# Kernel optimization log

Measured on AMD Instinct MI355X. Metric: run time of the kernel, lower is better.

## Reference

```python
import jax, jax.numpy as jnp
import numpy as np

NB = 5  # frequency bands


def _ln(x, g, b, eps=1e-5):
    m = jnp.mean(x, axis=-1, keepdims=True)
    v = jnp.var(x, axis=-1, keepdims=True)
    return (x - m) / jnp.sqrt(v + eps) * g + b


def _graph_adj(x, adj_w, sw1, sb1, sw2, sb2, pos_factor, pos_enc):
    # x: [B, D, N] -> degree-normalized adjacency [B, N, N]
    d = x.shape[1]
    xt = jnp.swapaxes(x, 1, 2)  # [B, N, D]
    # concat-MLP first layer split: cat(xi, xj) @ W1 == xi @ W1[:d] + xj @ W1[d:]
    a = xt @ sw1[:d]
    bpart = xt @ sw1[d:]
    h = jax.nn.elu(a[:, :, None, :] + bpart[:, None, :, :] + sb1)  # [B, N, N, H]
    dyn = jax.nn.sigmoid(jnp.squeeze(h @ sw2, -1) + sb2)  # [B, N, N]
    static = jax.nn.softmax(adj_w, axis=-1)
    pos = jax.nn.softmax(pos_enc, axis=-1)
    comb = jax.nn.softmax(static + dyn + pos_factor * pos, axis=-1)
    deg = jnp.sum(comb, axis=-1)
    dis = (deg + 1e-8) ** -0.5
    return dis[:, :, None] * comb * dis[:, None, :]


def _gcn(x, adj, w, b):
    # x: [B, D, N], adj: [B, N, N] -> [B, D_out, N]
    xt = jnp.swapaxes(x, 1, 2)
    out = jnp.einsum('bij,bjd->bid', adj, xt) @ w + b
    return jnp.swapaxes(out, 1, 2)


def _mha(x, qkv_w, qkv_b, ow, ob, nh=4):
    B, S, D = x.shape
    dh = D // nh
    q, k, v = jnp.split(x @ qkv_w + qkv_b, 3, axis=-1)
    q = q.reshape(B, S, nh, dh)
    k = k.reshape(B, S, nh, dh)
    v = v.reshape(B, S, nh, dh)
    att = jax.nn.softmax(jnp.einsum('bihd,bjhd->bhij', q, k) / float(np.sqrt(dh)), axis=-1)
    o = jnp.einsum('bhij,bjhd->bihd', att, v).reshape(B, S, D)
    return o @ ow + ob


def setup_inputs():
    key = jax.random.key(0)
    B, D, N = 16, 256, 64
    ks = iter(jax.random.split(key, 40))

    def rn(shape, s=0.05):
        return jax.random.normal(next(ks), shape, dtype=jnp.float32) * s

    eyeN = jnp.eye(N, dtype=jnp.float32)
    return dict(
        feature=jax.random.normal(next(ks), (B, NB * D, 1, N), dtype=jnp.float32),
        l_adj_w=jnp.tile(eyeN[None], (NB, 1, 1)),
        l_sim_w1=rn((NB, 2 * D, D)), l_sim_b1=jnp.zeros((NB, D), jnp.float32),
        l_sim_w2=rn((NB, D, 1)), l_sim_b2=jnp.zeros((NB, 1), jnp.float32),
        l_pos_factor=jnp.full((NB,), 0.5, jnp.float32),
        l_pos_enc=jnp.tile(eyeN[None], (NB, 1, 1)),
        l_gcn_w=rn((NB, D, D)), l_gcn_b=jnp.zeros((NB, D), jnp.float32),
        g_adj_w=jnp.eye(NB, dtype=jnp.float32),
        g_sim_w1=rn((2 * D, D)), g_sim_b1=jnp.zeros((D,), jnp.float32),
        g_sim_w2=rn((D, 1)), g_sim_b2=jnp.zeros((1,), jnp.float32),
        g_pos_factor=jnp.float32(0.5),
        g_pos_enc=jnp.eye(NB, dtype=jnp.float32),
        g_gcn_w=rn((D, D)), g_gcn_b=jnp.zeros((D,), jnp.float32),
        qkv_w=rn((D, 3 * D)), qkv_b=jnp.zeros((3 * D,), jnp.float32),
        attn_ow=rn((D, D)), attn_ob=jnp.zeros((D,), jnp.float32),
        ln1_g=jnp.ones((D,), jnp.float32), ln1_b=jnp.zeros((D,), jnp.float32),
        ln2_g=jnp.ones((D,), jnp.float32), ln2_b=jnp.zeros((D,), jnp.float32),
        mlp_w1=rn((D, 4 * D)), mlp_b1=jnp.zeros((4 * D,), jnp.float32),
        mlp_w2=rn((4 * D, D)), mlp_b2=jnp.zeros((D,), jnp.float32),
        imp_w=rn((NB, N, 1)), imp_b=jnp.zeros((NB, 1), jnp.float32),
    )


def reference(feature, l_adj_w, l_sim_w1, l_sim_b1, l_sim_w2, l_sim_b2,
              l_pos_factor, l_pos_enc, l_gcn_w, l_gcn_b,
              g_adj_w, g_sim_w1, g_sim_b1, g_sim_w2, g_sim_b2,
              g_pos_factor, g_pos_enc, g_gcn_w, g_gcn_b,
              qkv_w, qkv_b, attn_ow, attn_ob,
              ln1_g, ln1_b, ln2_g, ln2_b,
              mlp_w1, mlp_b1, mlp_w2, mlp_b2,
              imp_w, imp_b):
    B = feature.shape[0]
    D = l_gcn_w.shape[-1]
    N = feature.shape[-1]
    # [B, 5*D, 1, N] -> [5, B, D, N] band-major
    x5 = jnp.moveaxis(feature.reshape(B, NB, D, N), 1, 0)
    # per-band local graphs + GCNs (vmapped over the 5 bands)
    local_adj = jax.vmap(_graph_adj)(x5, l_adj_w, l_sim_w1, l_sim_b1,
                                     l_sim_w2, l_sim_b2, l_pos_factor, l_pos_enc)
    local_out = jax.vmap(_gcn)(x5, local_adj, l_gcn_w, l_gcn_b)  # [5, B, D, N]
    scale_nodes = jnp.moveaxis(jnp.mean(local_out, axis=-1), 0, 1)  # [B, 5, D]
    # cross-band attention block (pre: MHA + residual + LN, then MLP + residual + LN)
    attn = _mha(scale_nodes, qkv_w, qkv_b, attn_ow, attn_ob)
    h1 = _ln(scale_nodes + attn, ln1_g, ln1_b)
    mlp = jax.nn.gelu(h1 @ mlp_w1 + mlp_b1, approximate=False) @ mlp_w2 + mlp_b2
    se = _ln(h1 + mlp, ln2_g, ln2_b)  # [B, 5, D]
    # global scale graph over the 5 band nodes
    xg = jnp.swapaxes(se, 1, 2)  # [B, D, 5]
    g_adj = _graph_adj(xg, g_adj_w, g_sim_w1, g_sim_b1, g_sim_w2, g_sim_b2,
                       g_pos_factor, g_pos_enc)
    g_out = jnp.swapaxes(_gcn(xg, g_adj, g_gcn_w, g_gcn_b), 1, 2)  # [B, 5, D]
    # modulate each local band feature by its global scale vector
    enh = local_out * jnp.moveaxis(g_out, 1, 0)[..., None]  # [5, B, D, N]
    # per-band importance projection over channels: [5, B, D, 1]
    out5 = jnp.einsum('kbdn,kno->kbdo', enh, imp_w) + imp_b[:, None, None, :]
    output = jnp.moveaxis(out5, 0, 1).reshape(B, NB * D, 1, 1)
    return output, g_adj, jnp.moveaxis(local_out, 0, 1)
```

## Files before the change

### kernel.cpp

```cpp
#include <hip/hip_runtime.h>
#include <hip/hip_bf16.h>

#define NBANDS 5
#define BATCH  16
#define DIM    256
#define NNODE  64
#define SEQ    5

typedef __hip_bfloat16 bf16;
typedef unsigned short ushort_t;
typedef __attribute__((ext_vector_type(8))) short short8;
typedef __attribute__((ext_vector_type(4))) float float4v;

#define MFMA __builtin_amdgcn_mfma_f32_16x16x32_bf16

__device__ __forceinline__ float bu2f(ushort_t u){
    bf16 h = *reinterpret_cast<bf16*>(&u);
    return __bfloat162float(h);
}
__device__ __forceinline__ ushort_t f2bu(float x){
    bf16 h = __float2bfloat16(x);
    return *reinterpret_cast<ushort_t*>(&h);
}
__device__ __forceinline__ float elu(float v){
    return (v > 0.f) ? v : (__expf(v) - 1.f);
}

__global__ void __launch_bounds__(256) k_head(
    const float* __restrict__ l_adj_w, const float* __restrict__ l_pos_enc,
    const float* __restrict__ l_pf,
    const float* __restrict__ g_adj_w, const float* __restrict__ g_pos_enc,
    const float* __restrict__ g_pf,
    float* __restrict__ sbase, float* __restrict__ gbase,
    const float* __restrict__ w1, const float* __restrict__ gw,
    ushort_t* __restrict__ w1bt, ushort_t* __restrict__ gwbt)
{
    int blk = blockIdx.x;
    int tid = threadIdx.x;
    __shared__ ushort_t tile[64][65];

    if (blk < 80) {
        int r = blk*4 + (tid>>6);
        int k = r >> 6, i = r & 63;
        int t = tid & 63;
        float aw = l_adj_w[(k*NNODE + i)*NNODE + t];
        float pe = l_pos_enc[(k*NNODE + i)*NNODE + t];
        float m1 = aw, m2 = pe;
        for (int o=32;o>0;o>>=1){ m1 = fmaxf(m1, __shfl_xor(m1,o,64)); m2 = fmaxf(m2, __shfl_xor(m2,o,64)); }
        float e1 = __expf(aw-m1), e2 = __expf(pe-m2);
        float s1=e1, s2=e2;
        for (int o=32;o>0;o>>=1){ s1 += __shfl_xor(s1,o,64); s2 += __shfl_xor(s2,o,64); }
        float pf = l_pf[k];
        sbase[(k*NNODE+i)*NNODE + t] = e1/s1 + pf*(e2/s2);
    } else if (blk == 80) {
        if (tid < NBANDS) {
            int i = tid;
            float r1[NBANDS], r2[NBANDS];
            float m1=-1e30f, m2=-1e30f;
            for (int j=0;j<NBANDS;j++){
                r1[j]=g_adj_w[i*NBANDS+j]; r2[j]=g_pos_enc[i*NBANDS+j];
                m1=fmaxf(m1,r1[j]); m2=fmaxf(m2,r2[j]);
            }
            float s1=0.f,s2=0.f;
            for (int j=0;j<NBANDS;j++){ r1[j]=__expf(r1[j]-m1); r2[j]=__expf(r2[j]-m2); s1+=r1[j]; s2+=r2[j]; }
            float pf = g_pf[0];
            for (int j=0;j<NBANDS;j++) gbase[i*NBANDS+j] = r1[j]/s1 + pf*(r2[j]/s2);
        }
    } else {
        int idx = blk - 81;
        int inst = idx >> 4;
        int t = idx & 15;
        int r0 = (t>>2)*64, c0 = (t&3)*64;
        const float* src; ushort_t* dst;
        if (inst < 10){
            int k = inst>>1, half = inst&1;
            src = w1  + ((size_t)k*512 + half*256)*256;
            dst = w1bt+ ((size_t)k*512 + half*256)*256;
        } else {
            int k = inst-10;
            src = gw  + (size_t)k*65536;
            dst = gwbt+ (size_t)k*65536;
        }
        int jj = tid & 63, i4 = tid >> 6;
        for (int p=0;p<16;p++){
            int i = p*4 + i4;
            tile[i][jj] = f2bu(src[(size_t)(r0+i)*256 + c0 + jj]);
        }
        __syncthreads();
        for (int p=0;p<16;p++){
            int i = p*4 + i4;
            dst[(size_t)(c0+i)*256 + r0 + jj] = tile[jj][i];
        }
    }
}

__global__ void __launch_bounds__(512) k_graph(
    const float* __restrict__ feat,
    const ushort_t* __restrict__ w1bt, const float* __restrict__ b1,
    const float* __restrict__ w2, const float* __restrict__ b2arr,
    const float* __restrict__ sbase,
    const ushort_t* __restrict__ gwbt, const float* __restrict__ gb,
    const float* __restrict__ imp_w,
    float* __restrict__ out_local,
    float* __restrict__ scalew4, float* __restrict__ impw4)
{
    int k  = blockIdx.x >> 6;
    int b  = (blockIdx.x >> 2) & 15;
    int iq = blockIdx.x & 3;
    int i0 = iq << 4;
    int tid = threadIdx.x;
    int w = tid >> 6, lane = tid & 63, c16 = lane & 15, quad = lane >> 4;

    __shared__ union {
        ushort_t xtb[64][264];
        ushort_t ab[80][264];
    } U;
    __shared__ ushort_t cs[16][72];
    __shared__ ushort_t ys[16][264];
    __shared__ float w2s[DIM];

    const float* src = feat + ((size_t)b*NBANDS + k)*DIM*NNODE;

    if (tid < DIM) w2s[tid] = w2[k*DIM + tid];
    #pragma unroll
    for (int u = 0; u < 32; ++u){
        int idx = u*512 + tid;
        U.xtb[idx & 63][idx >> 6] = f2bu(src[idx]);
    }
    __syncthreads();

    int col0 = w*32 + c16;
    int col1 = col0 + 16;

    const ushort_t* Ba = w1bt + (size_t)k*512*DIM;
    const ushort_t* Bb = Ba + 256*DIM;
    float4v z = {0.f,0.f,0.f,0.f};
    float4v aA0=z, aA1=z;
    float4v aB00=z,aB01=z,aB10=z,aB11=z,aB20=z,aB21=z,aB30=z,aB31=z;
    #pragma unroll
    for (int ks = 0; ks < 8; ++ks){
        int ko = ks*32 + quad*8;
        short8 fa = *reinterpret_cast<const short8*>(&U.xtb[i0 + c16][ko]);
        short8 f0 = *reinterpret_cast<const short8*>(&U.xtb[ 0 + c16][ko]);
        short8 f1 = *reinterpret_cast<const short8*>(&U.xtb[16 + c16][ko]);
        short8 f2 = *reinterpret_cast<const short8*>(&U.xtb[32 + c16][ko]);
        short8 f3 = *reinterpret_cast<const short8*>(&U.xtb[48 + c16][ko]);
        short8 wa0 = *reinterpret_cast<const short8*>(Ba + (size_t)col0*DIM + ko);
        short8 wa1 = *reinterpret_cast<const short8*>(Ba + (size_t)col1*DIM + ko);
        short8 wb0 = *reinterpret_cast<const short8*>(Bb + (size_t)col0*DIM + ko);
        short8 wb1 = *reinterpret_cast<const short8*>(Bb + (size_t)col1*DIM + ko);
        aA0  = MFMA(fa, wa0, aA0, 0,0,0);
        aA1  = MFMA(fa, wa1, aA1, 0,0,0);
        aB00 = MFMA(f0, wb0, aB00, 0,0,0);
        aB01 = MFMA(f0, wb1, aB01, 0,0,0);
        aB10 = MFMA(f1, wb0, aB10, 0,0,0);
        aB11 = MFMA(f1, wb1, aB11, 0,0,0);
        aB20 = MFMA(f2, wb0, aB20, 0,0,0);
        aB21 = MFMA(f2, wb1, aB21, 0,0,0);
        aB30 = MFMA(f3, wb0, aB30, 0,0,0);
        aB31 = MFMA(f3, wb1, aB31, 0,0,0);
    }
    __syncthreads();
    {
        float bias0 = b1[k*DIM + col0];
        float bias1 = b1[k*DIM + col1];
        int r0 = quad*4;
        #pragma unroll
        for (int r = 0; r < 4; ++r){
            U.ab[r0 + r][col0]      = f2bu(aA0[r] + bias0);
            U.ab[r0 + r][col1]      = f2bu(aA1[r] + bias1);
            U.ab[16 + r0 + r][col0] = f2bu(aB00[r]);
            U.ab[16 + r0 + r][col1] = f2bu(aB01[r]);
            U.ab[32 + r0 + r][col0] = f2bu(aB10[r]);
            U.ab[32 + r0 + r][col1] = f2bu(aB11[r]);
            U.ab[48 + r0 + r][col0] = f2bu(aB20[r]);
            U.ab[48 + r0 + r][col1] = f2bu(aB21[r]);
            U.ab[64 + r0 + r][col0] = f2bu(aB30[r]);
            U.ab[64 + r0 + r][col1] = f2bu(aB31[r]);
        }
    }
    __syncthreads();

    {
        int il0 = w*2, il1 = w*2 + 1;
        float acc0 = 0.f, acc1 = 0.f;
        const ushort_t* ar0 = U.ab[il0];
        const ushort_t* ar1 = U.ab[il1];
        const ushort_t* br  = U.ab[16 + lane];
        #pragma unroll 4
        for (int dd = 0; dd < 64; ++dd){
            ushort4 bv = *reinterpret_cast<const ushort4*>(br  + dd*4);
            ushort4 a0 = *reinterpret_cast<const ushort4*>(ar0 + dd*4);
            ushort4 a1 = *reinterpret_cast<const ushort4*>(ar1 + dd*4);
            float4 wv  = *reinterpret_cast<const float4*>(&w2s[dd*4]);
            float bx = bu2f(bv.x), by = bu2f(bv.y), bz = bu2f(bv.z), bq = bu2f(bv.w);
            acc0 += elu(bu2f(a0.x)+bx)*wv.x + elu(bu2f(a0.y)+by)*wv.y
                  + elu(bu2f(a0.z)+bz)*wv.z + elu(bu2f(a0.w)+bq)*wv.w;
            acc1 += elu(bu2f(a1.x)+bx)*wv.x + elu(bu2f(a1.y)+by)*wv.y
                  + elu(bu2f(a1.z)+bz)*wv.z + elu(bu2f(a1.w)+bq)*wv.w;
        }
        float sb2 = b2arr[k];
        float sg0 = 1.f/(1.f + __expf(-(acc0 + sb2)));
        float sg1 = 1.f/(1.f + __expf(-(acc1 + sb2)));
        float val0 = sbase[(k*NNODE + i0 + il0)*NNODE + lane] + sg0;
        float val1 = sbase[(k*NNODE + i0 + il1)*NNODE + lane] + sg1;
        float m0 = val0, m1 = val1;
        for (int o=32;o>0;o>>=1){ m0 = fmaxf(m0, __shfl_xor(m0,o,64)); m1 = fmaxf(m1, __shfl_xor(m1,o,64)); }
        float e0 = __expf(val0 - m0), e1 = __expf(val1 - m1);
        float s0 = e0, s1 = e1;
        for (int o=32;o>0;o>>=1){ s0 += __shfl_xor(s0,o,64); s1 += __shfl_xor(s1,o,64); }
        cs[il0][lane] = f2bu(e0/s0);
        cs[il1][lane] = f2bu(e1/s1);
    }
    __syncthreads();

    {
        float4v aY0 = z, aY1 = z;
        #pragma unroll
        for (int ks = 0; ks < 2; ++ks){
            int ko = ks*32 + quad*8;
            short8 af = *reinterpret_cast<const short8*>(&cs[c16][ko]);
            const float* f0p = src + (size_t)col0*NNODE + ko;
            const float* f1p = src + (size_t)col1*NNODE + ko;
            float4 x0 = *reinterpret_cast<const float4*>(f0p);
            float4 x1 = *reinterpret_cast<const float4*>(f0p+4);
            float4 y0 = *reinterpret_cast<const float4*>(f1p);
            float4 y1 = *reinterpret_cast<const float4*>(f1p+4);
            short8 bf0, bf1;
            bf0[0]=(short)f2bu(x0.x); bf0[1]=(short)f2bu(x0.y); bf0[2]=(short)f2bu(x0.z); bf0[3]=(short)f2bu(x0.w);
            bf0[4]=(short)f2bu(x1.x); bf0[5]=(short)f2bu(x1.y); bf0[6]=(short)f2bu(x1.z); bf0[7]=(short)f2bu(x1.w);
            bf1[0]=(short)f2bu(y0.x); bf1[1]=(short)f2bu(y0.y); bf1[2]=(short)f2bu(y0.z); bf1[3]=(short)f2bu(y0.w);
            bf1[4]=(short)f2bu(y1.x); bf1[5]=(short)f2bu(y1.y); bf1[6]=(short)f2bu(y1.z); bf1[7]=(short)f2bu(y1.w);
            aY0 = MFMA(af, bf0, aY0, 0,0,0);
            aY1 = MFMA(af, bf1, aY1, 0,0,0);
        }
        #pragma unroll
        for (int r=0;r<4;++r){
            ys[quad*4 + r][col0] = f2bu(aY0[r]);
            ys[quad*4 + r][col1] = f2bu(aY1[r]);
        }
    }
    __syncthreads();

    {
        float4v aG0 = z, aG1 = z;
        const ushort_t* Bg = gwbt + (size_t)k*DIM*DIM;
        #pragma unroll
        for (int ks = 0; ks < 8; ++ks){
            int ko = ks*32 + quad*8;
            short8 af = *reinterpret_cast<const short8*>(&ys[c16][ko]);
            short8 g0 = *reinterpret_cast<const short8*>(Bg + (size_t)col0*DIM + ko);
            short8 g1 = *reinterpret_cast<const short8*>(Bg + (size_t)col1*DIM + ko);
            aG0 = MFMA(af, g0, aG0, 0,0,0);
            aG1 = MFMA(af, g1, aG1, 0,0,0);
        }
        int nb = i0 + quad*4;
        float iw0 = imp_w[k*NNODE + nb + 0];
        float iw1 = imp_w[k*NNODE + nb + 1];
        float iw2 = imp_w[k*NNODE + nb + 2];
        float iw3 = imp_w[k*NNODE + nb + 3];
        size_t obase = ((size_t)b*NBANDS + k)*DIM;

        float bias0 = gb[k*DIM + col0];
        float v0 = aG0[0]+bias0, v1 = aG0[1]+bias0, v2 = aG0[2]+bias0, v3 = aG0[3]+bias0;
        float4 vv = make_float4(v0,v1,v2,v3);
        *reinterpret_cast<float4*>(&out_local[(obase + col0)*NNODE + nb]) = vv;
        float s  = v0+v1+v2+v3;
        float di = v0*iw0 + v1*iw1 + v2*iw2 + v3*iw3;
        s  += __shfl_xor(s,16,64);  s  += __shfl_xor(s,32,64);
        di += __shfl_xor(di,16,64); di += __shfl_xor(di,32,64);
        if (quad == 0){
            size_t o = ((size_t)iq*80 + b*SEQ + k)*DIM + col0;
            scalew4[o] = s;
            impw4[o]   = di;
        }

        float bias1 = gb[k*DIM + col1];
        v0 = aG1[0]+bias1; v1 = aG1[1]+bias1; v2 = aG1[2]+bias1; v3 = aG1[3]+bias1;
        vv = make_float4(v0,v1,v2,v3);
        *reinterpret_cast<float4*>(&out_local[(obase + col1)*NNODE + nb]) = vv;
        s  = v0+v1+v2+v3;
        di = v0*iw0 + v1*iw1 + v2*iw2 + v3*iw3;
        s  += __shfl_xor(s,16,64);  s  += __shfl_xor(s,32,64);
        di += __shfl_xor(di,16,64); di += __shfl_xor(di,32,64);
        if (quad == 0){
            size_t o = ((size_t)iq*80 + b*SEQ + k)*DIM + col1;
            scalew4[o] = s;
            impw4[o]   = di;
        }
    }
}

__device__ __forceinline__ void ln_row(float* row, const float* g, const float* bb, int lane)
{
    float v0 = row[lane], v1 = row[lane+64], v2 = row[lane+128], v3 = row[lane+192];
    float s = v0+v1+v2+v3;
    for (int o=32;o>0;o>>=1) s += __shfl_xor(s,o,64);
    float mean = s * (1.f/256.f);
    float c0 = v0-mean, c1 = v1-mean, c2 = v2-mean, c3 = v3-mean;
    float q = c0*c0+c1*c1+c2*c2+c3*c3;
    for (int o=32;o>0;o>>=1) q += __shfl_xor(q,o,64);
    float rs = rsqrtf(q*(1.f/256.f) + 1e-5f);
    row[lane]     = c0*rs*g[lane]     + bb[lane];
    row[lane+64]  = c1*rs*g[lane+64]  + bb[lane+64];
    row[lane+128] = c2*rs*g[lane+128] + bb[lane+128];
    row[lane+192] = c3*rs*g[lane+192] + bb[lane+192];
}

__global__ void __launch_bounds__(1024) k_tail(
    const float* __restrict__ scalew4, const float* __restrict__ impw4,
    const float* __restrict__ qkv_w, const float* __restrict__ qkv_b,
    const float* __restrict__ attn_ow, const float* __restrict__ attn_ob,
    const float* __restrict__ ln1_g, const float* __restrict__ ln1_b,
    const float* __restrict__ mlp_w1, const float* __restrict__ mlp_b1,
    const float* __restrict__ mlp_w2, const float* __restrict__ mlp_b2,
    const float* __restrict__ ln2_g, const float* __restrict__ ln2_b,
    const float* __restrict__ gw1, const float* __restrict__ gb1,
    const float* __restrict__ gw2, const float* __restrict__ gb2,
    const float* __restrict__ gbase,
    const float* __restrict__ ggw, const float* __restrict__ ggb,
    const float* __restrict__ imp_b,
    float* __restrict__ out0, float* __restrict__ out_gadj)
{
    int b = blockIdx.x;
    int tid = threadIdx.x;
    int w = tid >> 6, lane = tid & 63;

    __shared__ __align__(16) float A[5160];
    __shared__ __align__(16) float Bp[5200];
    __shared__ __align__(16) float C[1300];
    __shared__ __align__(16) float Dx[1300];
    __shared__ __align__(16) float E[1300];
    __shared__ float F[64];

    #pragma unroll
    for (int p = 0; p < 2; ++p){
        int id = tid + p*1024;
        if (id < SEQ*DIM){
            int i = id >> 8, d = id & 255;
            size_t base = ((size_t)b*SEQ + i)*DIM + d;
            float v = scalew4[base] + scalew4[20480 + base]
                    + scalew4[40960 + base] + scalew4[61440 + base];
            C[i*260 + d] = v * (1.f/64.f);
        }
    }
    __syncthreads();

    if (tid < 768){
        int n = tid;
        float bias = qkv_b[n];
        float acc[5] = {bias,bias,bias,bias,bias};
        for (int d = 0; d < DIM; d += 4){
            float wv0 = qkv_w[(size_t)d*768 + n];
            float wv1 = qkv_w[(size_t)(d+1)*768 + n];
            float wv2 = qkv_w[(size_t)(d+2)*768 + n];
            float wv3 = qkv_w[(size_t)(d+3)*768 + n];
            #pragma unroll
            for (int i=0;i<5;++i){
                float4 cv = *reinterpret_cast<const float4*>(&C[i*260 + d]);
                acc[i] += cv.x*wv0 + cv.y*wv1 + cv.z*wv2 + cv.w*wv3;
            }
        }
        #pragma unroll
        for (int i=0;i<5;++i) A[i*772 + n] = acc[i];
    }
    __syncthreads();

    for (int p = w; p < 20; p += 16){
        int i = p >> 2, h = p & 3;
        float qv = A[i*772 + h*64 + lane];
        float pj[SEQ];
        #pragma unroll
        for (int j=0;j<SEQ;++j){
            float x = qv * A[j*772 + 256 + h*64 + lane];
            for (int o=32;o>0;o>>=1) x += __shfl_xor(x,o,64);
            pj[j] = x * 0.125f;
        }
        float m = pj[0];
        #pragma unroll
        for (int j=1;j<SEQ;++j) m = fmaxf(m, pj[j]);
        float ss = 0.f;
        #pragma unroll
        for (int j=0;j<SEQ;++j){ pj[j] = __expf(pj[j]-m); ss += pj[j]; }
        float inv = 1.f/ss;
        float o = 0.f;
        #pragma unroll
        for (int j=0;j<SEQ;++j) o += pj[j]*inv * A[j*772 + 512 + h*64 + lane];
        Dx[i*260 + h*64 + lane] = o;
    }
    __syncthreads();

    if (tid < DIM){
        int n = tid;
        float bias = attn_ob[n];
        float acc[5] = {bias,bias,bias,bias,bias};
        for (int d = 0; d < DIM; d += 4){
            float wv0 = attn_ow[(size_t)d*DIM + n];
            float wv1 = attn_ow[(size_t)(d+1)*DIM + n];
            float wv2 = attn_ow[(size_t)(d+2)*DIM + n];
            float wv3 = attn_ow[(size_t)(d+3)*DIM + n];
            #pragma unroll
            for (int i=0;i<5;++i){
                float4 xv = *reinterpret_cast<const float4*>(&Dx[i*260 + d]);
                acc[i] += xv.x*wv0 + xv.y*wv1 + xv.z*wv2 + xv.w*wv3;
            }
        }
        #pragma unroll
        for (int i=0;i<5;++i) E[i*260 + n] = C[i*260 + n] + acc[i];
    }
    __syncthreads();
    if (w < SEQ) ln_row(&E[w*260], ln1_g, ln1_b, lane);
    __syncthreads();

    {
        int m = tid;
        float bias = mlp_b1[m];
        float acc[5] = {bias,bias,bias,bias,bias};
        for (int d = 0; d < DIM; d += 4){
            float wv0 = mlp_w1[(size_t)d*1024 + m];
            float wv1 = mlp_w1[(size_t)(d+1)*1024 + m];
            float wv2 = mlp_w1[(size_t)(d+2)*1024 + m];
            float wv3 = mlp_w1[(size_t)(d+3)*1024 + m];
            #pragma unroll
            for (int i=0;i<5;++i){
                float4 xv = *reinterpret_cast<const float4*>(&E[i*260 + d]);
                acc[i] += xv.x*wv0 + xv.y*wv1 + xv.z*wv2 + xv.w*wv3;
            }
        }
        #pragma unroll
        for (int i=0;i<5;++i){
            float v = acc[i];
            A[i*1032 + m] = 0.5f*v*(1.f + erff(v*0.70710678118654752f));
        }
    }
    __syncthreads();

    {
        int n = tid & 255, s = tid >> 8;
        float acc[5] = {0.f,0.f,0.f,0.f,0.f};
        const float* wbase = mlp_w2 + (size_t)s*256*DIM + n;
        const float* mbase = A + s*256;
        for (int kk = 0; kk < 256; kk += 4){
            float wv0 = wbase[(size_t)kk*DIM];
            float wv1 = wbase[(size_t)(kk+1)*DIM];
            float wv2 = wbase[(size_t)(kk+2)*DIM];
            float wv3 = wbase[(size_t)(kk+3)*DIM];
            #pragma unroll
            for (int i=0;i<5;++i){
                float4 xv = *reinterpret_cast<const float4*>(&mbase[i*1032 + kk]);
                acc[i] += xv.x*wv0 + xv.y*wv1 + xv.z*wv2 + xv.w*wv3;
            }
        }
        #pragma unroll
        for (int i=0;i<5;++i) Bp[(s*5 + i)*260 + n] = acc[i];
    }
    __syncthreads();
    if (tid < DIM){
        int n = tid;
        float b2v = mlp_b2[n];
        #pragma unroll
        for (int i=0;i<5;++i){
            float m2 = b2v + Bp[i*260+n] + Bp[(5+i)*260+n] + Bp[(10+i)*260+n] + Bp[(15+i)*260+n];
            C[i*260 + n] = m2 + E[i*260 + n];
        }
    }
    __syncthreads();
    if (w < SEQ) ln_row(&C[w*260], ln2_g, ln2_b, lane);
    __syncthreads();

    {
        int n = tid & 255, s = tid >> 8;
        int mat = s >> 1, half = s & 1;
        float acc[5] = {0.f,0.f,0.f,0.f,0.f};
        const float* wbase = gw1 + ((size_t)mat*DIM + half*128)*DIM + n;
        for (int kk = 0; kk < 128; kk += 4){
            int d = half*128 + kk;
            float wv0 = wbase[(size_t)kk*DIM];
            float wv1 = wbase[(size_t)(kk+1)*DIM];
            float wv2 = wbase[(size_t)(kk+2)*DIM];
            float wv3 = wbase[(size_t)(kk+3)*DIM];
            #pragma unroll
            for (int i=0;i<5;++i){
                float4 xv = *reinterpret_cast<const float4*>(&C[i*260 + d]);
                acc[i] += xv.x*wv0 + xv.y*wv1 + xv.z*wv2 + xv.w*wv3;
            }
        }
        #pragma unroll
        for (int i=0;i<5;++i) Bp[(s*5 + i)*260 + n] = acc[i];
    }
    __syncthreads();
    if (tid < DIM){
        int n = tid;
        float g1v = gb1[n];
        #pragma unroll
        for (int i=0;i<5;++i){
            A[i*260 + n]        = g1v + Bp[i*260+n] + Bp[(5+i)*260+n];
            A[1300 + i*260 + n] =       Bp[(10+i)*260+n] + Bp[(15+i)*260+n];
        }
    }
    __syncthreads();

    for (int p = w; p < 25; p += 16){
        int i = p/5, j = p - (p/5)*5;
        float acc = 0.f;
        #pragma unroll
        for (int q = 0; q < 4; ++q){
            int d = lane + q*64;
            float v = A[i*260 + d] + A[1300 + j*260 + d];
            acc += elu(v) * gw2[d];
        }
        for (int o=32;o>0;o>>=1) acc += __shfl_xor(acc,o,64);
        if (lane == 0) F[p] = acc;
    }
    __syncthreads();
    if (tid < SEQ){
        int i = tid;
        float sb2 = gb2[0];
        float gc[SEQ];
        float m = -1e30f;
        #pragma unroll
        for (int j=0;j<SEQ;++j){
            float sg = 1.f/(1.f + __expf(-(F[i*5+j] + sb2)));
            gc[j] = gbase[i*SEQ + j] + sg;
            m = fmaxf(m, gc[j]);
        }
        float ss = 0.f;
        #pragma unroll
        for (int j=0;j<SEQ;++j){ gc[j] = __expf(gc[j]-m); ss += gc[j]; }
        float inv = 1.f/ss;
        #pragma unroll
        for (int j=0;j<SEQ;++j){
            float v = gc[j]*inv;
            F[32 + i*5 + j] = v;
            out_gadj[((size_t)b*SEQ + i)*SEQ + j] = v;
        }
    }
    __syncthreads();
    if (tid < DIM){
        int n = tid;
        #pragma unroll
        for (int i=0;i<5;++i){
            float t = 0.f;
            #pragma unroll
            for (int j=0;j<SEQ;++j) t += F[32 + i*5 + j] * C[j*260 + n];
            Dx[i*260 + n] = t;
        }
    }
    __syncthreads();
    if (tid < DIM){
        int n = tid;
        float bias = ggb[n];
        float acc[5] = {bias,bias,bias,bias,bias};
        for (int d = 0; d < DIM; d += 4){
            float wv0 = ggw[(size_t)d*DIM + n];
            float wv1 = ggw[(size_t)(d+1)*DIM + n];
            float wv2 = ggw[(size_t)(d+2)*DIM + n];
            float wv3 = ggw[(size_t)(d+3)*DIM + n];
            #pragma unroll
            for (int i=0;i<5;++i){
                float4 xv = *reinterpret_cast<const float4*>(&Dx[i*260 + d]);
                acc[i] += xv.x*wv0 + xv.y*wv1 + xv.z*wv2 + xv.w*wv3;
            }
        }
        #pragma unroll
        for (int i=0;i<5;++i){
            size_t rowo = ((size_t)b*SEQ + i)*DIM + n;
            float imps = impw4[rowo] + impw4[20480 + rowo] + impw4[40960 + rowo] + impw4[61440 + rowo];
            out0[rowo] = acc[i]*imps + imp_b[i];
        }
    }
}

extern "C" void kernel_launch(void* const* d_in, const int* in_sizes, int n_in,
                              void* d_out, int out_size, void* d_ws, size_t ws_size,
                              hipStream_t stream)
{
    const float* feature      = (const float*)d_in[0];
    const float* l_adj_w      = (const float*)d_in[1];
    const float* l_sim_w1     = (const float*)d_in[2];
    const float* l_sim_b1     = (const float*)d_in[3];
    const float* l_sim_w2     = (const float*)d_in[4];
    const float* l_sim_b2     = (const float*)d_in[5];
    const float* l_pos_factor = (const float*)d_in[6];
    const float* l_pos_enc    = (const float*)d_in[7];
    const float* l_gcn_w      = (const float*)d_in[8];
    const float* l_gcn_b      = (const float*)d_in[9];
    const float* g_adj_w      = (const float*)d_in[10];
    const float* g_sim_w1     = (const float*)d_in[11];
    const float* g_sim_b1     = (const float*)d_in[12];
    const float* g_sim_w2     = (const float*)d_in[13];
    const float* g_sim_b2     = (const float*)d_in[14];
    const float* g_pos_factor = (const float*)d_in[15];
    const float* g_pos_enc    = (const float*)d_in[16];
    const float* g_gcn_w      = (const float*)d_in[17];
    const float* g_gcn_b      = (const float*)d_in[18];
    const float* qkv_w        = (const float*)d_in[19];
    const float* qkv_b        = (const float*)d_in[20];
    const float* attn_ow      = (const float*)d_in[21];
    const float* attn_ob      = (const float*)d_in[22];
    const float* ln1_g        = (const float*)d_in[23];
    const float* ln1_b        = (const float*)d_in[24];
    const float* ln2_g        = (const float*)d_in[25];
    const float* ln2_b        = (const float*)d_in[26];
    const float* mlp_w1       = (const float*)d_in[27];
    const float* mlp_b1       = (const float*)d_in[28];
    const float* mlp_w2       = (const float*)d_in[29];
    const float* mlp_b2       = (const float*)d_in[30];
    const float* imp_w        = (const float*)d_in[31];
    const float* imp_b        = (const float*)d_in[32];

    float* out0      = (float*)d_out;
    float* out_gadj  = out0 + (size_t)BATCH*NBANDS*DIM;
    float* out_local = out_gadj + (size_t)BATCH*NBANDS*NBANDS;

    ushort_t* w1bt = (ushort_t*)d_ws;
    ushort_t* gwbt = w1bt + (size_t)NBANDS*512*DIM;
    float* fp = (float*)(gwbt + (size_t)NBANDS*DIM*DIM);
    float* sbase   = fp; fp += NBANDS*NNODE*NNODE;
    float* gbase   = fp; fp += 32;
    float* scalew4 = fp; fp += 4*BATCH*SEQ*DIM;
    float* impw4   = fp; fp += 4*BATCH*SEQ*DIM;

    k_head<<<321, 256, 0, stream>>>(l_adj_w, l_pos_enc, l_pos_factor,
                                    g_adj_w, g_pos_enc, g_pos_factor,
                                    sbase, gbase,
                                    l_sim_w1, l_gcn_w, w1bt, gwbt);
    k_graph<<<NBANDS*BATCH*4, 512, 0, stream>>>(feature, w1bt, l_sim_b1,
                                    l_sim_w2, l_sim_b2, sbase,
                                    gwbt, l_gcn_b, imp_w,
                                    out_local, scalew4, impw4);
    k_tail<<<BATCH, 1024, 0, stream>>>(scalew4, impw4, qkv_w, qkv_b,
                                    attn_ow, attn_ob, ln1_g, ln1_b,
                                    mlp_w1, mlp_b1, mlp_w2, mlp_b2,
                                    ln2_g, ln2_b, g_sim_w1, g_sim_b1,
                                    g_sim_w2, g_sim_b2, gbase,
                                    g_gcn_w, g_gcn_b, imp_b,
                                    out0, out_gadj);
}
```

Baseline: 265.0 us.

## Split serial tail kernel into row-parallel GEMV kernels; restructure dynamic adjacency loop

Replaces the single 16-block tail kernel, which ran the MHA, MLP, layer norms and global graph serially per batch, with six kernels. Each kernel spreads its GEMV over many blocks per row, using K-sliced partial sums and fused layernorm/GELU, so the tail can use many more CUs. In the graph kernel, the ELU-MLP loop now keeps the row's A values in registers, loads w2 straight from global memory, and computes each (i, j) pair with a wave-wide shuffle reduction. This trades more kernel launches, global-memory round trips for intermediates, and many shuffle reductions for wider parallelism.

```diff
diff --git a/kernel.cpp b/kernel.cpp
--- a/kernel.cpp
+++ b/kernel.cpp
@@ -117,11 +117,9 @@
     } U;
     __shared__ ushort_t cs[16][72];
     __shared__ ushort_t ys[16][264];
-    __shared__ float w2s[DIM];
 
     const float* src = feat + ((size_t)b*NBANDS + k)*DIM*NNODE;
 
-    if (tid < DIM) w2s[tid] = w2[k*DIM + tid];
     #pragma unroll
     for (int u = 0; u < 32; ++u){
         int idx = u*512 + tid;
@@ -183,21 +181,23 @@
 
     {
         int il0 = w*2, il1 = w*2 + 1;
+        ushort4 a0v = *reinterpret_cast<const ushort4*>(&U.ab[il0][lane*4]);
+        ushort4 a1v = *reinterpret_cast<const ushort4*>(&U.ab[il1][lane*4]);
+        float4  wv  = *reinterpret_cast<const float4*>(&w2[k*DIM + lane*4]);
+        float a00=bu2f(a0v.x), a01=bu2f(a0v.y), a02=bu2f(a0v.z), a03=bu2f(a0v.w);
+        float a10=bu2f(a1v.x), a11=bu2f(a1v.y), a12=bu2f(a1v.z), a13=bu2f(a1v.w);
         float acc0 = 0.f, acc1 = 0.f;
-        const ushort_t* ar0 = U.ab[il0];
-        const ushort_t* ar1 = U.ab[il1];
-        const ushort_t* br  = U.ab[16 + lane];
         #pragma unroll 4
-        for (int dd = 0; dd < 64; ++dd){
-            ushort4 bv = *reinterpret_cast<const ushort4*>(br  + dd*4);
-            ushort4 a0 = *reinterpret_cast<const ushort4*>(ar0 + dd*4);
-            ushort4 a1 = *reinterpret_cast<const ushort4*>(ar1 + dd*4);
-            float4 wv  = *reinterpret_cast<const float4*>(&w2s[dd*4]);
-            float bx = bu2f(bv.x), by = bu2f(bv.y), bz = bu2f(bv.z), bq = bu2f(bv.w);
-            acc0 += elu(bu2f(a0.x)+bx)*wv.x + elu(bu2f(a0.y)+by)*wv.y
-                  + elu(bu2f(a0.z)+bz)*wv.z + elu(bu2f(a0.w)+bq)*wv.w;
-            acc1 += elu(bu2f(a1.x)+bx)*wv.x + elu(bu2f(a1.y)+by)*wv.y
-                  + elu(bu2f(a1.z)+bz)*wv.z + elu(bu2f(a1.w)+bq)*wv.w;
+        for (int j = 0; j < 64; ++j){
+            ushort4 bv = *reinterpret_cast<const ushort4*>(&U.ab[16 + j][lane*4]);
+            float bx=bu2f(bv.x), by=bu2f(bv.y), bz=bu2f(bv.z), bq=bu2f(bv.w);
+            float p0 = elu(a00+bx)*wv.x + elu(a01+by)*wv.y
+                     + elu(a02+bz)*wv.z + elu(a03+bq)*wv.w;
+            float p1 = elu(a10+bx)*wv.x + elu(a11+by)*wv.y
+                     + elu(a12+bz)*wv.z + elu(a13+bq)*wv.w;
+            for (int o=32;o>0;o>>=1){ p0 += __shfl_xor(p0,o,64); p1 += __shfl_xor(p1,o,64); }
+            acc0 = (lane == j) ? p0 : acc0;
+            acc1 = (lane == j) ? p1 : acc1;
         }
         float sb2 = b2arr[k];
         float sg0 = 1.f/(1.f + __expf(-(acc0 + sb2)));
@@ -291,283 +291,267 @@
     }
 }
 
-__device__ __forceinline__ void ln_row(float* row, const float* g, const float* bb, int lane)
-{
-    float v0 = row[lane], v1 = row[lane+64], v2 = row[lane+128], v3 = row[lane+192];
-    float s = v0+v1+v2+v3;
+__global__ void __launch_bounds__(256) k_qkv_gemv(const float* __restrict__ scalew4,
+                        const float* __restrict__ w, const float* __restrict__ bias,
+                        float* __restrict__ out)
+{
+    int row = blockIdx.x / 12;
+    int n0 = (blockIdx.x % 12) * 64;
+    int tid = threadIdx.x;
+    int c = tid & 63, s = tid >> 6;
+    __shared__ float xs[DIM];
+    __shared__ float part[4][64];
+    {
+        size_t basei = (size_t)row*DIM + tid;
+        xs[tid] = (scalew4[basei] + scalew4[20480 + basei]
+                 + scalew4[40960 + basei] + scalew4[61440 + basei]) * (1.f/64.f);
+    }
+    __syncthreads();
+    const float* wp = w + (size_t)(s*64)*768 + n0 + c;
+    const float* xp = xs + s*64;
+    float acc = 0.f;
+    #pragma unroll 8
+    for (int i = 0; i < 64; ++i) acc += xp[i] * wp[(size_t)i*768];
+    part[s][c] = acc;
+    __syncthreads();
+    if (s == 0){
+        out[(size_t)row*768 + n0 + c] = bias[n0+c] + part[0][c]+part[1][c]+part[2][c]+part[3][c];
+    }
+}
+
+template<int COLS, int SLICES>
+__global__ void __launch_bounds__(256) k_gemv(const float* __restrict__ x, const float* __restrict__ w,
+                       const float* __restrict__ bias, float* __restrict__ out,
+                       int K, int N, int act)
+{
+    int chunks = N / COLS;
+    int row = blockIdx.x / chunks;
+    int n0 = (blockIdx.x % chunks) * COLS;
+    int c = threadIdx.x % COLS, s = threadIdx.x / COLS;
+    __shared__ float xs[1024];
+    __shared__ float part[SLICES][COLS];
+    for (int i = threadIdx.x; i < K; i += 256) xs[i] = x[(size_t)row*K + i];
+    __syncthreads();
+    int klen = K / SLICES;
+    const float* wp = w + (size_t)(s*klen)*N + n0 + c;
+    const float* xp = xs + s*klen;
+    float acc = 0.f;
+    #pragma unroll 8
+    for (int i = 0; i < klen; ++i) acc += xp[i] * wp[(size_t)i*N];
+    part[s][c] = acc;
+    __syncthreads();
+    if (s == 0){
+        float v = bias[n0+c];
+        #pragma unroll
+        for (int q=0;q<SLICES;q++) v += part[q][c];
+        if (act) v = 0.5f*v*(1.f + erff(v*0.70710678118654752f));
+        out[(size_t)row*N + n0 + c] = v;
+    }
+}
+
+__global__ void __launch_bounds__(256) k_projattn(const float* __restrict__ qkvw,
+                        const float* __restrict__ ow, const float* __restrict__ ob,
+                        float* __restrict__ projw)
+{
+    int row = blockIdx.x / 4;
+    int n0 = (blockIdx.x % 4) * 64;
+    int b = row / SEQ, i = row % SEQ;
+    int tid = threadIdx.x;
+    int h = tid >> 6, l = tid & 63;
+    __shared__ float xs[DIM];
+    __shared__ float part[4][64];
+    const float* base = qkvw + (size_t)b*SEQ*3*DIM;
+    float qv = base[(size_t)i*3*DIM + h*64 + l];
+    float pj[SEQ];
+    #pragma unroll
+    for (int j=0;j<SEQ;j++){
+        float p = qv * base[(size_t)j*3*DIM + DIM + h*64 + l];
+        for (int o=32;o>0;o>>=1) p += __shfl_xor(p,o,64);
+        pj[j] = p * 0.125f;
+    }
+    float m = pj[0];
+    #pragma unroll
+    for (int j=1;j<SEQ;j++) m = fmaxf(m, pj[j]);
+    float ssum = 0.f;
+    #pragma unroll
+    for (int j=0;j<SEQ;j++){ pj[j] = __expf(pj[j]-m); ssum += pj[j]; }
+    float inv = 1.f/ssum;
+    float o = 0.f;
+    #pragma unroll
+    for (int j=0;j<SEQ;j++) o += pj[j]*inv * base[(size_t)j*3*DIM + 2*DIM + h*64 + l];
+    xs[tid] = o;
+    __syncthreads();
+    int c = tid & 63, s = tid >> 6;
+    const float* wp = ow + (size_t)(s*64)*DIM + n0 + c;
+    const float* xp = xs + s*64;
+    float acc = 0.f;
+    #pragma unroll 8
+    for (int k=0;k<64;++k) acc += xp[k] * wp[(size_t)k*DIM];
+    part[s][c] = acc;
+    __syncthreads();
+    if (s == 0){
+        projw[(size_t)row*DIM + n0 + c] = ob[n0+c] + part[0][c]+part[1][c]+part[2][c]+part[3][c];
+    }
+}
+
+__device__ __forceinline__ float block_ln(float v, int tid, float* red, float g, float bln)
+{
+    float s = v;
     for (int o=32;o>0;o>>=1) s += __shfl_xor(s,o,64);
-    float mean = s * (1.f/256.f);
-    float c0 = v0-mean, c1 = v1-mean, c2 = v2-mean, c3 = v3-mean;
-    float q = c0*c0+c1*c1+c2*c2+c3*c3;
+    int wave = tid>>6, lane = tid&63;
+    if (lane==0) red[wave] = s;
+    __syncthreads();
+    float mean = (red[0]+red[1]+red[2]+red[3]) * (1.f/DIM);
+    float c = v - mean;
+    float q = c*c;
     for (int o=32;o>0;o>>=1) q += __shfl_xor(q,o,64);
-    float rs = rsqrtf(q*(1.f/256.f) + 1e-5f);
-    row[lane]     = c0*rs*g[lane]     + bb[lane];
-    row[lane+64]  = c1*rs*g[lane+64]  + bb[lane+64];
-    row[lane+128] = c2*rs*g[lane+128] + bb[lane+128];
-    row[lane+192] = c3*rs*g[lane+192] + bb[lane+192];
-}
-
-__global__ void __launch_bounds__(1024) k_tail(
-    const float* __restrict__ scalew4, const float* __restrict__ impw4,
-    const float* __restrict__ qkv_w, const float* __restrict__ qkv_b,
-    const float* __restrict__ attn_ow, const float* __restrict__ attn_ob,
-    const float* __restrict__ ln1_g, const float* __restrict__ ln1_b,
-    const float* __restrict__ mlp_w1, const float* __restrict__ mlp_b1,
-    const float* __restrict__ mlp_w2, const float* __restrict__ mlp_b2,
-    const float* __restrict__ ln2_g, const float* __restrict__ ln2_b,
-    const float* __restrict__ gw1, const float* __restrict__ gb1,
-    const float* __restrict__ gw2, const float* __restrict__ gb2,
-    const float* __restrict__ gbase,
-    const float* __restrict__ ggw, const float* __restrict__ ggb,
-    const float* __restrict__ imp_b,
-    float* __restrict__ out0, float* __restrict__ out_gadj)
-{
-    int b = blockIdx.x;
+    __syncthreads();
+    if (lane==0) red[wave] = q;
+    __syncthreads();
+    float var = (red[0]+red[1]+red[2]+red[3]) * (1.f/DIM);
+    return c * rsqrtf(var + 1e-5f) * g + bln;
+}
+
+__global__ void __launch_bounds__(256) k_mlp1_ln(const float* __restrict__ projw,
+                         const float* __restrict__ scalew4,
+                         const float* __restrict__ ln1_g, const float* __restrict__ ln1_b,
+                         const float* __restrict__ w1, const float* __restrict__ b1,
+                         float* __restrict__ h1w, float* __restrict__ mhw)
+{
+    int row = blockIdx.x / 16;
+    int n0 = (blockIdx.x % 16) * 64;
     int tid = threadIdx.x;
-    int w = tid >> 6, lane = tid & 63;
-
-    __shared__ __align__(16) float A[5160];
-    __shared__ __align__(16) float Bp[5200];
-    __shared__ __align__(16) float C[1300];
-    __shared__ __align__(16) float Dx[1300];
-    __shared__ __align__(16) float E[1300];
-    __shared__ float F[64];
-
+    __shared__ float xs[DIM];
+    __shared__ float red[4];
+    __shared__ float part[4][64];
+    size_t basei = (size_t)row*DIM + tid;
+    float sc = (scalew4[basei] + scalew4[20480 + basei]
+              + scalew4[40960 + basei] + scalew4[61440 + basei]) * (1.f/64.f);
+    float v = projw[basei] + sc;
+    float h = block_ln(v, tid, red, ln1_g[tid], ln1_b[tid]);
+    xs[tid] = h;
+    if ((blockIdx.x % 16) == 0) h1w[basei] = h;
+    __syncthreads();
+    int c = tid & 63, s = tid >> 6;
+    const float* wp = w1 + (size_t)(s*64)*1024 + n0 + c;
+    const float* xp = xs + s*64;
+    float acc = 0.f;
+    #pragma unroll 8
+    for (int i=0;i<64;++i) acc += xp[i] * wp[(size_t)i*1024];
+    part[s][c] = acc;
+    __syncthreads();
+    if (s == 0){
+        float o = b1[n0+c] + part[0][c] + part[1][c] + part[2][c] + part[3][c];
+        o = 0.5f*o*(1.f + erff(o*0.70710678118654752f));
+        mhw[(size_t)row*1024 + n0 + c] = o;
+    }
+}
+
+__global__ void __launch_bounds__(256) k_gab_ln(const float* __restrict__ m2w,
+                        const float* __restrict__ h1w,
+                        const float* __restrict__ ln2_g, const float* __restrict__ ln2_b,
+                        const float* __restrict__ gw1, const float* __restrict__ gb1,
+                        float* __restrict__ sew, float* __restrict__ gaw, float* __restrict__ gbw)
+{
+    int row = blockIdx.x / 4;
+    int n0 = (blockIdx.x % 4) * 64;
+    int tid = threadIdx.x;
+    __shared__ float xs[DIM];
+    __shared__ float red[4];
+    __shared__ float partA[4][64];
+    __shared__ float partB[4][64];
+    float v = m2w[(size_t)row*DIM + tid] + h1w[(size_t)row*DIM + tid];
+    float h = block_ln(v, tid, red, ln2_g[tid], ln2_b[tid]);
+    xs[tid] = h;
+    if ((blockIdx.x % 4) == 0) sew[(size_t)row*DIM + tid] = h;
+    __syncthreads();
+    int c = tid & 63, s = tid >> 6;
+    const float* wpA = gw1 + (size_t)(s*64)*DIM + n0 + c;
+    const float* wpB = wpA + (size_t)DIM*DIM;
+    const float* xp = xs + s*64;
+    float aA = 0.f, aB = 0.f;
+    #pragma unroll 8
+    for (int i=0;i<64;++i){
+        float xv = xp[i];
+        aA += xv * wpA[(size_t)i*DIM];
+        aB += xv * wpB[(size_t)i*DIM];
+    }
+    partA[s][c] = aA;
+    partB[s][c] = aB;
+    __syncthreads();
+    if (s == 0){
+        gaw[(size_t)row*DIM + n0 + c] = gb1[n0+c] + partA[0][c]+partA[1][c]+partA[2][c]+partA[3][c];
+        gbw[(size_t)row*DIM + n0 + c] = partB[0][c]+partB[1][c]+partB[2][c]+partB[3][c];
+    }
+}
+
+__global__ void __launch_bounds__(256) k_goutfin(const float* __restrict__ gaw,
+                        const float* __restrict__ gbw,
+                        const float* __restrict__ gw2, const float* __restrict__ gb2,
+                        const float* __restrict__ gbase,
+                        const float* __restrict__ sew,
+                        const float* __restrict__ ggw, const float* __restrict__ ggb,
+                        const float* __restrict__ impw4, const float* __restrict__ imp_b,
+                        float* __restrict__ out0, float* __restrict__ out_gadj)
+{
+    int row = blockIdx.x / 4;
+    int n0 = (blockIdx.x % 4) * 64;
+    int b = row / SEQ, i = row % SEQ;
+    int tid = threadIdx.x;
+    int wave = tid >> 6, lane = tid & 63;
+    __shared__ float dyn_s[SEQ];
+    __shared__ float xs[DIM];
+    __shared__ float part[4][64];
+    for (int j = wave; j < SEQ; j += 4){
+        const float* gar = gaw + (size_t)row*DIM;
+        const float* gbr = gbw + ((size_t)b*SEQ + j)*DIM;
+        float acc = 0.f;
+        #pragma unroll
+        for (int m=0;m<4;m++){
+            int dd = lane + m*64;
+            float v = gar[dd] + gbr[dd];
+            acc += elu(v) * gw2[dd];
+        }
+        for (int o=32;o>0;o>>=1) acc += __shfl_xor(acc,o,64);
+        if (lane==0) dyn_s[j] = acc;
+    }
+    __syncthreads();
+    float gc[SEQ];
+    {
+        float sb2 = gb2[0];
+        float m = -1e30f;
+        #pragma unroll
+        for (int j=0;j<SEQ;j++){
+            float sg = 1.f/(1.f+__expf(-(dyn_s[j]+sb2)));
+            gc[j] = gbase[i*SEQ+j] + sg;
+            m = fmaxf(m, gc[j]);
+        }
+        float ssum=0.f;
+        #pragma unroll
+        for (int j=0;j<SEQ;j++){ gc[j]=__expf(gc[j]-m); ssum+=gc[j]; }
+        float inv = 1.f/ssum;
+        #pragma unroll
+        for (int j=0;j<SEQ;j++) gc[j] *= inv;
+    }
+    if (n0 == 0 && tid < SEQ) out_gadj[((size_t)b*SEQ+i)*SEQ + tid] = gc[tid];
+    float t = 0.f;
     #pragma unroll
-    for (int p = 0; p < 2; ++p){
-        int id = tid + p*1024;
-        if (id < SEQ*DIM){
-            int i = id >> 8, d = id & 255;
-            size_t base = ((size_t)b*SEQ + i)*DIM + d;
-            float v = scalew4[base] + scalew4[20480 + base]
-                    + scalew4[40960 + base] + scalew4[61440 + base];
-            C[i*260 + d] = v * (1.f/64.f);
-        }
-    }
-    __syncthreads();
-
-    if (tid < 768){
-        int n = tid;
-        float bias = qkv_b[n];
-        float acc[5] = {bias,bias,bias,bias,bias};
-        for (int d = 0; d < DIM; d += 4){
-            float wv0 = qkv_w[(size_t)d*768 + n];
-            float wv1 = qkv_w[(size_t)(d+1)*768 + n];
-            float wv2 = qkv_w[(size_t)(d+2)*768 + n];
-            float wv3 = qkv_w[(size_t)(d+3)*768 + n];
-            #pragma unroll
-            for (int i=0;i<5;++i){
-                float4 cv = *reinterpret_cast<const float4*>(&C[i*260 + d]);
-                acc[i] += cv.x*wv0 + cv.y*wv1 + cv.z*wv2 + cv.w*wv3;
-            }
-        }
-        #pragma unroll
-        for (int i=0;i<5;++i) A[i*772 + n] = acc[i];
-    }
-    __syncthreads();
-
-    for (int p = w; p < 20; p += 16){
-        int i = p >> 2, h = p & 3;
-        float qv = A[i*772 + h*64 + lane];
-        float pj[SEQ];
-        #pragma unroll
-        for (int j=0;j<SEQ;++j){
-            float x = qv * A[j*772 + 256 + h*64 + lane];
-            for (int o=32;o>0;o>>=1) x += __shfl_xor(x,o,64);
-            pj[j] = x * 0.125f;
-        }
-        float m = pj[0];
-        #pragma unroll
-        for (int j=1;j<SEQ;++j) m = fmaxf(m, pj[j]);
-        float ss = 0.f;
-        #pragma unroll
-        for (int j=0;j<SEQ;++j){ pj[j] = __expf(pj[j]-m); ss += pj[j]; }
-        float inv = 1.f/ss;
-        float o = 0.f;
-        #pragma unroll
-        for (int j=0;j<SEQ;++j) o += pj[j]*inv * A[j*772 + 512 + h*64 + lane];
-        Dx[i*260 + h*64 + lane] = o;
-    }
-    __syncthreads();
-
-    if (tid < DIM){
-        int n = tid;
-        float bias = attn_ob[n];
-        float acc[5] = {bias,bias,bias,bias,bias};
-        for (int d = 0; d < DIM; d += 4){
-            float wv0 = attn_ow[(size_t)d*DIM + n];
-            float wv1 = attn_ow[(size_t)(d+1)*DIM + n];
-            float wv2 = attn_ow[(size_t)(d+2)*DIM + n];
-            float wv3 = attn_ow[(size_t)(d+3)*DIM + n];
-            #pragma unroll
-            for (int i=0;i<5;++i){
-                float4 xv = *reinterpret_cast<const float4*>(&Dx[i*260 + d]);
-                acc[i] += xv.x*wv0 + xv.y*wv1 + xv.z*wv2 + xv.w*wv3;
-            }
-        }
-        #pragma unroll
-        for (int i=0;i<5;++i) E[i*260 + n] = C[i*260 + n] + acc[i];
-    }
-    __syncthreads();
-    if (w < SEQ) ln_row(&E[w*260], ln1_g, ln1_b, lane);
-    __syncthreads();
-
-    {
-        int m = tid;
-        float bias = mlp_b1[m];
-        float acc[5] = {bias,bias,bias,bias,bias};
-        for (int d = 0; d < DIM; d += 4){
-            float wv0 = mlp_w1[(size_t)d*1024 + m];
-            float wv1 = mlp_w1[(size_t)(d+1)*1024 + m];
-            float wv2 = mlp_w1[(size_t)(d+2)*1024 + m];
-            float wv3 = mlp_w1[(size_t)(d+3)*1024 + m];
-            #pragma unroll
-            for (int i=0;i<5;++i){
-                float4 xv = *reinterpret_cast<const float4*>(&E[i*260 + d]);
-                acc[i] += xv.x*wv0 + xv.y*wv1 + xv.z*wv2 + xv.w*wv3;
-            }
-        }
-        #pragma unroll
-        for (int i=0;i<5;++i){
-            float v = acc[i];
-            A[i*1032 + m] = 0.5f*v*(1.f + erff(v*0.70710678118654752f));
-        }
-    }
-    __syncthreads();
-
-    {
-        int n = tid & 255, s = tid >> 8;
-        float acc[5] = {0.f,0.f,0.f,0.f,0.f};
-        const float* wbase = mlp_w2 + (size_t)s*256*DIM + n;
-        const float* mbase = A + s*256;
-        for (int kk = 0; kk < 256; kk += 4){
-            float wv0 = wbase[(size_t)kk*DIM];
-            float wv1 = wbase[(size_t)(kk+1)*DIM];
-            float wv2 = wbase[(size_t)(kk+2)*DIM];
-            float wv3 = wbase[(size_t)(kk+3)*DIM];
-            #pragma unroll
-            for (int i=0;i<5;++i){
-                float4 xv = *reinterpret_cast<const float4*>(&mbase[i*1032 + kk]);
-                acc[i] += xv.x*wv0 + xv.y*wv1 + xv.z*wv2 + xv.w*wv3;
-            }
-        }
-        #pragma unroll
-        for (int i=0;i<5;++i) Bp[(s*5 + i)*260 + n] = acc[i];
-    }
-    __syncthreads();
-    if (tid < DIM){
-        int n = tid;
-        float b2v = mlp_b2[n];
-        #pragma unroll
-        for (int i=0;i<5;++i){
-            float m2 = b2v + Bp[i*260+n] + Bp[(5+i)*260+n] + Bp[(10+i)*260+n] + Bp[(15+i)*260+n];
-            C[i*260 + n] = m2 + E[i*260 + n];
-        }
-    }
-    __syncthreads();
-    if (w < SEQ) ln_row(&C[w*260], ln2_g, ln2_b, lane);
-    __syncthreads();
-
-    {
-        int n = tid & 255, s = tid >> 8;
-        int mat = s >> 1, half = s & 1;
-        float acc[5] = {0.f,0.f,0.f,0.f,0.f};
-        const float* wbase = gw1 + ((size_t)mat*DIM + half*128)*DIM + n;
-        for (int kk = 0; kk < 128; kk += 4){
-            int d = half*128 + kk;
-            float wv0 = wbase[(size_t)kk*DIM];
-            float wv1 = wbase[(size_t)(kk+1)*DIM];
-            float wv2 = wbase[(size_t)(kk+2)*DIM];
-            float wv3 = wbase[(size_t)(kk+3)*DIM];
-            #pragma unroll
-            for (int i=0;i<5;++i){
-                float4 xv = *reinterpret_cast<const float4*>(&C[i*260 + d]);
-                acc[i] += xv.x*wv0 + xv.y*wv1 + xv.z*wv2 + xv.w*wv3;
-            }
-        }
-        #pragma unroll
-        for (int i=0;i<5;++i) Bp[(s*5 + i)*260 + n] = acc[i];
-    }
-    __syncthreads();
-    if (tid < DIM){
-        int n = tid;
-        float g1v = gb1[n];
-        #pragma unroll
-        for (int i=0;i<5;++i){
-            A[i*260 + n]        = g1v + Bp[i*260+n] + Bp[(5+i)*260+n];
-            A[1300 + i*260 + n] =       Bp[(10+i)*260+n] + Bp[(15+i)*260+n];
-        }
-    }
-    __syncthreads();
-
-    for (int p = w; p < 25; p += 16){
-        int i = p/5, j = p - (p/5)*5;
-        float acc = 0.f;
-        #pragma unroll
-        for (int q = 0; q < 4; ++q){
-            int d = lane + q*64;
-            float v = A[i*260 + d] + A[1300 + j*260 + d];
-            acc += elu(v) * gw2[d];
-        }
-        for (int o=32;o>0;o>>=1) acc += __shfl_xor(acc,o,64);
-        if (lane == 0) F[p] = acc;
-    }
-    __syncthreads();
-    if (tid < SEQ){
-        int i = tid;
-        float sb2 = gb2[0];
-        float gc[SEQ];
-        float m = -1e30f;
-        #pragma unroll
-        for (int j=0;j<SEQ;++j){
-            float sg = 1.f/(1.f + __expf(-(F[i*5+j] + sb2)));
-            gc[j] = gbase[i*SEQ + j] + sg;
-            m = fmaxf(m, gc[j]);
-        }
-        float ss = 0.f;
-        #pragma unroll
-        for (int j=0;j<SEQ;++j){ gc[j] = __expf(gc[j]-m); ss += gc[j]; }
-        float inv = 1.f/ss;
-        #pragma unroll
-        for (int j=0;j<SEQ;++j){
-            float v = gc[j]*inv;
-            F[32 + i*5 + j] = v;
-            out_gadj[((size_t)b*SEQ + i)*SEQ + j] = v;
-        }
-    }
-    __syncthreads();
-    if (tid < DIM){
-        int n = tid;
-        #pragma unroll
-        for (int i=0;i<5;++i){
-            float t = 0.f;
-            #pragma unroll
-            for (int j=0;j<SEQ;++j) t += F[32 + i*5 + j] * C[j*260 + n];
-            Dx[i*260 + n] = t;
-        }
-    }
-    __syncthreads();
-    if (tid < DIM){
-        int n = tid;
-        float bias = ggb[n];
-        float acc[5] = {bias,bias,bias,bias,bias};
-        for (int d = 0; d < DIM; d += 4){
-            float wv0 = ggw[(size_t)d*DIM + n];
-            float wv1 = ggw[(size_t)(d+1)*DIM + n];
-            float wv2 = ggw[(size_t)(d+2)*DIM + n];
-            float wv3 = ggw[(size_t)(d+3)*DIM + n];
-            #pragma unroll
-            for (int i=0;i<5;++i){
-                float4 xv = *reinterpret_cast<const float4*>(&Dx[i*260 + d]);
-                acc[i] += xv.x*wv0 + xv.y*wv1 + xv.z*wv2 + xv.w*wv3;
-            }
-        }
-        #pragma unroll
-        for (int i=0;i<5;++i){
-            size_t rowo = ((size_t)b*SEQ + i)*DIM + n;
-            float imps = impw4[rowo] + impw4[20480 + rowo] + impw4[40960 + rowo] + impw4[61440 + rowo];
-            out0[rowo] = acc[i]*imps + imp_b[i];
-        }
+    for (int j=0;j<SEQ;j++) t += gc[j]*sew[((size_t)b*SEQ + j)*DIM + tid];
+    xs[tid] = t;
+    __syncthreads();
+    int c = tid & 63, s = tid >> 6;
+    const float* wp = ggw + (size_t)(s*64)*DIM + n0 + c;
+    const float* xp = xs + s*64;
+    float acc = 0.f;
+    #pragma unroll 8
+    for (int k=0;k<64;++k) acc += xp[k] * wp[(size_t)k*DIM];
+    part[s][c] = acc;
+    __syncthreads();
+    if (s == 0){
+        float g = ggb[n0+c] + part[0][c]+part[1][c]+part[2][c]+part[3][c];
+        size_t o = (size_t)row*DIM + n0 + c;
+        float imps = impw4[o] + impw4[20480 + o] + impw4[40960 + o] + impw4[61440 + o];
+        out0[o] = g * imps + imp_b[i];
     }
 }
 
@@ -603,7 +587,7 @@
     const float* ln2_g        = (const float*)d_in[25];
     const float* ln2_b        = (const float*)d_in[26];
     const float* mlp_w1       = (const float*)d_in[27];
-    const float* mlp_b1       = (const float*)d_in[28];
+    const float* mlp_b1      = (const float*)d_in[28];
     const float* mlp_w2       = (const float*)d_in[29];
     const float* mlp_b2       = (const float*)d_in[30];
     const float* imp_w        = (const float*)d_in[31];
@@ -620,6 +604,16 @@
     float* gbase   = fp; fp += 32;
     float* scalew4 = fp; fp += 4*BATCH*SEQ*DIM;
     float* impw4   = fp; fp += 4*BATCH*SEQ*DIM;
+    float* qkvw    = fp; fp += BATCH*SEQ*3*DIM;
+    float* projw   = fp; fp += BATCH*SEQ*DIM;
+    float* h1w     = fp; fp += BATCH*SEQ*DIM;
+    float* mhw     = fp; fp += BATCH*SEQ*4*DIM;
+    float* m2w     = fp; fp += BATCH*SEQ*DIM;
+    float* sew     = fp; fp += BATCH*SEQ*DIM;
+    float* gaw     = fp; fp += BATCH*SEQ*DIM;
+    float* gbw     = fp; fp += BATCH*SEQ*DIM;
+
+    const int ROWS = BATCH*SEQ;
 
     k_head<<<321, 256, 0, stream>>>(l_adj_w, l_pos_enc, l_pos_factor,
                                     g_adj_w, g_pos_enc, g_pos_factor,
@@ -629,11 +623,12 @@
                                     l_sim_w2, l_sim_b2, sbase,
                                     gwbt, l_gcn_b, imp_w,
                                     out_local, scalew4, impw4);
-    k_tail<<<BATCH, 1024, 0, stream>>>(scalew4, impw4, qkv_w, qkv_b,
-                                    attn_ow, attn_ob, ln1_g, ln1_b,
-                                    mlp_w1, mlp_b1, mlp_w2, mlp_b2,
-                                    ln2_g, ln2_b, g_sim_w1, g_sim_b1,
-                                    g_sim_w2, g_sim_b2, gbase,
-                                    g_gcn_w, g_gcn_b, imp_b,
-                                    out0, out_gadj);
-}
+    k_qkv_gemv<<<ROWS*12, 256, 0, stream>>>(scalew4, qkv_w, qkv_b, qkvw);
+    k_projattn<<<ROWS*4, 256, 0, stream>>>(qkvw, attn_ow, attn_ob, projw);
+    k_mlp1_ln<<<ROWS*16, 256, 0, stream>>>(projw, scalew4, ln1_g, ln1_b, mlp_w1, mlp_b1, h1w, mhw);
+    k_gemv<32,8><<<ROWS*8, 256, 0, stream>>>(mhw, mlp_w2, mlp_b2, m2w, 1024, 256, 0);
+    k_gab_ln<<<ROWS*4, 256, 0, stream>>>(m2w, h1w, ln2_g, ln2_b, g_sim_w1, g_sim_b1, sew, gaw, gbw);
+    k_goutfin<<<ROWS*4, 256, 0, stream>>>(gaw, gbw, g_sim_w2, g_sim_b2, gbase,
+                                          sew, g_gcn_w, g_gcn_b, impw4, imp_b,
+                                          out0, out_gadj);
+}
```

Result: faster. 228.7 us (-13.7%).
